# Kernel tuning notes

Hardware: AMD Instinct MI355X
Metric: run time of the kernel (lower is better)

The kernel has to match this reference:

```python
import jax, jax.numpy as jnp
import numpy as np

M, NQ, NKV, DX, DT = 8, 1024, 1024, 512, 2
H, HD = 8, 64            # num_heads, head_dim
INNER = H * HD           # 512
KHID = 16                # kernel MLP hidden dim
SCALE = HD ** -0.5


def setup_inputs() -> dict:
    key = jax.random.key(0)
    ks = jax.random.split(key, 16)
    s = lambda fan_in: 1.0 / np.sqrt(fan_in)
    return {
        "xq": jax.random.normal(ks[0], (M, NQ, DX), jnp.float32),
        "xk": jax.random.normal(ks[1], (M, NKV, DX), jnp.float32),
        "xv": jax.random.normal(ks[2], (M, NKV, DX), jnp.float32),
        "tq": jax.random.normal(ks[3], (M, NQ, DT), jnp.float32),
        "tk": jax.random.normal(ks[4], (M, NKV, DT), jnp.float32),
        # attention projections (bias=False for q/k/v, Linear bias for out)
        "w_q": jax.random.normal(ks[5], (DX, INNER), jnp.float32) * s(DX),
        "w_k": jax.random.normal(ks[6], (DX, INNER), jnp.float32) * s(DX),
        "w_v": jax.random.normal(ks[7], (DX, INNER), jnp.float32) * s(DX),
        "w_out": jax.random.normal(ks[8], (INNER, DX), jnp.float32) * s(INNER),
        "b_out": jnp.zeros((DX,), jnp.float32),
        # kernel MLP: dt -> KHID -> H (per-head pairwise bias)
        "kw1": jax.random.normal(ks[9], (DT, KHID), jnp.float32) * s(DT),
        "kb1": jnp.zeros((KHID,), jnp.float32),
        "kw2": jax.random.normal(ks[10], (KHID, H), jnp.float32) * s(KHID),
        "kb2": jnp.zeros((H,), jnp.float32),
    }


def reference(xq, xk, xv, tq, tk, w_q, w_k, w_v, w_out, b_out, kw1, kb1, kw2, kb2):
    # pairwise differences of input locations: [m, nq, nkv, dt]
    diff = tq[:, :, None, :] - tk[:, None, :, :]
    # kernel MLP -> per-head bias, rearranged to [m, h, nq, nkv]
    hmid = jax.nn.relu(diff @ kw1 + kb1)          # [m, nq, nkv, KHID]
    dots = jnp.einsum('mqkc,ch->mhqk', hmid, kw2) + kb2[None, :, None, None]
    # token attention: standard scaled QK scores
    q = (xq @ w_q).reshape(M, NQ, H, HD)          # [m, nq, h, d]
    k = (xk @ w_k).reshape(M, NKV, H, HD)
    token_dots = jnp.einsum('mqhd,mkhd->mhqk', q, k) * SCALE
    dots = dots + token_dots
    attn = jax.nn.softmax(dots, axis=-1)          # softmax over keys
    v = (xv @ w_v).reshape(M, NKV, H, HD)
    out = jnp.einsum('mhqk,mkhd->mqhd', attn, v).reshape(M, NQ, INNER)
    return out @ w_out + b_out                    # [m, nq, dx]
```

## Files before the change

kernel.cpp:

```cpp
#include <hip/hip_runtime.h>


typedef unsigned short u16;
typedef unsigned int   u32;
typedef short bf8 __attribute__((ext_vector_type(8)));
typedef float f4  __attribute__((ext_vector_type(4)));
typedef _Float16 h2 __attribute__((ext_vector_type(2)));

#define Mb 8
#define LOG2E 1.44269504088896f
#define SCALE2 (0.125f * LOG2E)
#define NTOK 4194304

__device__ __forceinline__ u16 f2bf(float f) {
    union { float f; u32 u; } v; v.f = f;
    u32 r = v.u + 0x7fffu + ((v.u >> 16) & 1u);
    return (u16)(r >> 16);
}
__device__ __forceinline__ u32 pk2(float a, float b) {
    u32 r;
    asm("v_cvt_pk_bf16_f32 %0, %1, %2" : "=v"(r) : "v"(a), "v"(b));
    return r;
}
__device__ __forceinline__ void gl_lds16(const u16* g, u16* l) {
    __builtin_amdgcn_global_load_lds(
        (const __attribute__((address_space(1))) u32*)g,
        (__attribute__((address_space(3))) u32*)l, 16, 0, 0);
}
__device__ __forceinline__ h2 h2_of(u32 x) {
    union { u32 u; h2 h; } c; c.u = x; return c.h;
}
__device__ __forceinline__ u32 u_of(h2 x) {
    union { h2 h; u32 u; } c; c.h = x; return c.u;
}
__device__ __forceinline__ float dot2(h2 a, h2 b, float c) {
#if __has_builtin(__builtin_amdgcn_fdot2)
    return __builtin_amdgcn_fdot2(a, b, c, false);
#else
    return fmaf((float)a[0], (float)b[0], fmaf((float)a[1], (float)b[1], c));
#endif
}

struct PArgs {
    const float* ws[4];
    u16* dstW;
};

__global__ __launch_bounds__(256) void prep(PArgs p) {
    __shared__ u16 tl[64][80];
    const int tid = threadIdx.x;
    const int bb = blockIdx.x;
    const int mat = bb >> 6, t = bb & 63;
    const int kt = t >> 3, nt = t & 7;
    const float* src = p.ws[mat] + (size_t)kt * 64 * 512 + (size_t)nt * 64;
    const int r0 = tid >> 4, c4 = (tid & 15) * 4;
    #pragma unroll
    for (int rr = 0; rr < 4; ++rr) {
        const int row = r0 + rr * 16;
        float4 a = *(const float4*)(src + (size_t)row * 512 + c4);
        tl[c4 + 0][row] = f2bf(a.x);
        tl[c4 + 1][row] = f2bf(a.y);
        tl[c4 + 2][row] = f2bf(a.z);
        tl[c4 + 3][row] = f2bf(a.w);
    }
    __syncthreads();
    u16* dst = p.dstW + (size_t)mat * 262144 + (size_t)nt * 64 * 512 + (size_t)kt * 64;
    #pragma unroll
    for (int i = 0; i < 2; ++i) {
        const int s2 = tid + i * 256;
        const int nrow = s2 >> 3, k8 = (s2 & 7) * 8;
        *(uint4*)(dst + (size_t)nrow * 512 + k8) = *(const uint4*)&tl[nrow][k8];
    }
}

struct GArgs {
    const void*  A[3];
    const u16*   W[3];
    void*        C[3];
    const float* bias;
    int          modeT[3];
    int          outf32;
    int          af32;
};

__global__ __launch_bounds__(256) void gemm_mfma(GArgs g) {
    __shared__ u16 Xs[128][32];
    __shared__ u16 Ws[128][32];

    const int z   = blockIdx.z;
    const int tid = threadIdx.x;
    const int w = tid >> 6, lane = tid & 63, quad = lane >> 4, l16 = lane & 15;
    const int wm = w >> 1, wn = w & 1;
    const int n0 = blockIdx.x * 128, t0 = blockIdx.y * 128;
    const int trans = g.modeT[z];

    f4 acc[4][4];
    #pragma unroll
    for (int i = 0; i < 4; ++i)
        #pragma unroll
        for (int j = 0; j < 4; ++j) acc[i][j] = (f4)0.f;

    const int lrow  = lane >> 2;
    const int kslot = (lane & 3) ^ ((lane >> 3) & 3);
    u16* ldsW0 = &Ws[w * 32][0];
    u16* ldsW1 = &Ws[w * 32 + 16][0];
    const u16* gW0 = g.W[z] + (size_t)(n0 + w * 32 + lrow) * 512 + kslot * 8;
    const u16* gW1 = gW0 + 16 * 512;

    u16* ldsX0 = &Xs[w * 32][0];
    u16* ldsX1 = &Xs[w * 32 + 16][0];
    const u16* gA0 = (const u16*)g.A[z] + (size_t)(t0 + w * 32 + lrow) * 512 + kslot * 8;
    const u16* gA1 = gA0 + 16 * 512;
    const int arow_s = tid >> 1, ah = tid & 1;
    const float* aF = (const float*)g.A[z] + (size_t)(t0 + arow_s) * 512 + ah * 16;
    const int s_sw = (arow_s >> 1) & 3;
    u16* aw0 = &Xs[arow_s][((2 * ah)     ^ s_sw) * 8];
    u16* aw1 = &Xs[arow_s][((2 * ah + 1) ^ s_sw) * 8];

    const int rslot = (quad ^ ((l16 >> 1) & 3)) * 8;

    for (int kc = 0; kc < 512; kc += 32) {
        __syncthreads();
        if (g.af32) {
            float4 f0 = *(const float4*)(aF + kc);
            float4 f1 = *(const float4*)(aF + kc + 4);
            float4 f2 = *(const float4*)(aF + kc + 8);
            float4 f3 = *(const float4*)(aF + kc + 12);
            uint4 v0, v1;
            v0.x = pk2(f0.x, f0.y); v0.y = pk2(f0.z, f0.w);
            v0.z = pk2(f1.x, f1.y); v0.w = pk2(f1.z, f1.w);
            v1.x = pk2(f2.x, f2.y); v1.y = pk2(f2.z, f2.w);
            v1.z = pk2(f3.x, f3.y); v1.w = pk2(f3.z, f3.w);
            *(uint4*)aw0 = v0;
            *(uint4*)aw1 = v1;
        } else {
            gl_lds16(gA0 + kc, ldsX0);
            gl_lds16(gA1 + kc, ldsX1);
        }
        gl_lds16(gW0 + kc, ldsW0);
        gl_lds16(gW1 + kc, ldsW1);
        __syncthreads();

        const u16* Abase = trans ? &Xs[0][0] : &Ws[0][0];
        const u16* Bbase = trans ? &Ws[0][0] : &Xs[0][0];
        const int arow = (trans ? wm : wn) * 64;
        const int brow = (trans ? wn : wm) * 64;
        bf8 af[4], bf[4];
        #pragma unroll
        for (int i = 0; i < 4; ++i)
            af[i] = *(const bf8*)(Abase + (arow + i * 16 + l16) * 32 + rslot);
        #pragma unroll
        for (int j = 0; j < 4; ++j)
            bf[j] = *(const bf8*)(Bbase + (brow + j * 16 + l16) * 32 + rslot);
        #pragma unroll
        for (int i = 0; i < 4; ++i)
            #pragma unroll
            for (int j = 0; j < 4; ++j)
                acc[i][j] = __builtin_amdgcn_mfma_f32_16x16x32_bf16(af[i], bf[j], acc[i][j], 0, 0, 0);
    }

    if (g.outf32) {
        float* Co = (float*)g.C[z];
        #pragma unroll
        for (int i = 0; i < 4; ++i) {
            const int nb = n0 + wn * 64 + i * 16 + quad * 4;
            float4 bv = *(const float4*)&g.bias[nb];
            #pragma unroll
            for (int j = 0; j < 4; ++j) {
                const int tok = t0 + wm * 64 + j * 16 + l16;
                float4 st;
                st.x = acc[i][j][0] + bv.x; st.y = acc[i][j][1] + bv.y;
                st.z = acc[i][j][2] + bv.z; st.w = acc[i][j][3] + bv.w;
                *(float4*)&Co[(size_t)tok * 512 + nb] = st;
            }
        }
    } else if (!trans) {
        u16* C = (u16*)g.C[z];
        #pragma unroll
        for (int i = 0; i < 4; ++i) {
            const int nb = n0 + wn * 64 + i * 16 + quad * 4;
            #pragma unroll
            for (int j = 0; j < 4; ++j) {
                const int tok = t0 + wm * 64 + j * 16 + l16;
                uint2 pw;
                pw.x = pk2(acc[i][j][0], acc[i][j][1]);
                pw.y = pk2(acc[i][j][2], acc[i][j][3]);
                *(uint2*)&C[(size_t)tok * 512 + nb] = pw;
            }
        }
    } else {
        u16* Vt = (u16*)g.C[z];
        #pragma unroll
        for (int i = 0; i < 4; ++i) {
            const int tokb = t0 + wm * 64 + i * 16 + quad * 4;
            const int mb = tokb >> 10, tb = tokb & 1023;
            #pragma unroll
            for (int j = 0; j < 4; ++j) {
                const int n = n0 + wn * 64 + j * 16 + l16;
                uint2 pw;
                pw.x = pk2(acc[i][j][0], acc[i][j][1]);
                pw.y = pk2(acc[i][j][2], acc[i][j][3]);
                *(uint2*)&Vt[(size_t)mb * 524288 + (size_t)n * 1024 + tb] = pw;
            }
        }
    }
}

__global__ __launch_bounds__(512) void attn_mfma(
    const u16* __restrict__ Q, const u16* __restrict__ K,
    const u16* __restrict__ Vt,
    const float* __restrict__ tqp, const float* __restrict__ tkp,
    const float* __restrict__ kw1, const float* __restrict__ kb1,
    const float* __restrict__ kw2,
    u16* __restrict__ O)
{
    __shared__ u16 sK[2][8][64][8];
    __shared__ u16 sV[2][8][64][8];
    __shared__ u32 sv2[2][8][68];
    __shared__ u16 sP[8][16][68];

    const int tid = threadIdx.x;
    const int w = tid >> 6, lane = tid & 63, quad = lane >> 4, l16 = lane & 15;
    const int b = (blockIdx.z * 8 + blockIdx.y) * 8 + blockIdx.x;
    const int xc = b & 7, j = b >> 3;
    const int hm = xc * 8 + (j & 7);
    const int qt = j >> 3;
    const int h = hm & 7, m = hm >> 3;
    const int q0 = qt * 128;
    const size_t qtok = (size_t)m * 1024 + q0 + w * 16 + l16;

    bf8 qf[2];
    {
        const u16* qp = Q + qtok * 512 + h * 64 + quad * 8;
        qf[0] = *(const bf8*)qp;
        qf[1] = *(const bf8*)(qp + 32);
    }
    h2 u2[8], w2p[8];
    {
        const float t0v = tqp[qtok * 2], t1v = tqp[qtok * 2 + 1];
        #pragma unroll
        for (int cp = 0; cp < 8; ++cp) {
            const int c0 = 2 * cp, c1 = 2 * cp + 1;
            float ua = fmaf(t0v, kw1[c0], fmaf(t1v, kw1[16 + c0], kb1[c0]));
            float ub = fmaf(t0v, kw1[c1], fmaf(t1v, kw1[16 + c1], kb1[c1]));
            u2[cp][0]  = (_Float16)ua;  u2[cp][1]  = (_Float16)ub;
            w2p[cp][0] = (_Float16)(LOG2E * kw2[c0 * 8 + h]);
            w2p[cp][1] = (_Float16)(LOG2E * kw2[c1 * 8 + h]);
        }
    }
    const float w0a = kw1[2 * w],     w1a = kw1[16 + 2 * w];
    const float w0b = kw1[2 * w + 1], w1b = kw1[16 + 2 * w + 1];

    const u16* gK = K + ((size_t)m * 1024 + lane) * 512 + h * 64 + w * 8;
    const u16* gV = Vt + (size_t)m * 524288 + (size_t)(h * 64 + lane) * 1024 + w * 8;
    const float* gT = tkp + (size_t)m * 2048 + lane * 2;

    float mrun = -1e30f, lrun = 0.f;
    f4 o[4];
    #pragma unroll
    for (int d = 0; d < 4; ++d) o[d] = (f4)0.f;

    auto STAGE = [&](int kt2, int nb) {
        const int k0n = kt2 * 64;
        float2 t = *(const float2*)(gT + k0n * 2);
        h2 pv;
        pv[0] = (_Float16)fmaf(t.x, w0a, t.y * w1a);
        pv[1] = (_Float16)fmaf(t.x, w0b, t.y * w1b);
        sv2[nb][w][lane] = u_of(pv);
        gl_lds16(gK + (size_t)k0n * 512, &sK[nb][w][0][0]);
        gl_lds16(gV + k0n,               &sV[nb][w][0][0]);
    };

    STAGE(0, 0);
    __syncthreads();

    int cur = 0;
    for (int kt = 0; kt < 16; ++kt) {
        if (kt < 15) STAGE(kt + 1, cur ^ 1);

        f4 s[4];
        #pragma unroll
        for (int msub = 0; msub < 4; ++msub) {
            bf8 kf0 = *(const bf8*)&sK[cur][quad][msub * 16 + l16][0];
            bf8 kf1 = *(const bf8*)&sK[cur][4 + quad][msub * 16 + l16][0];
            s[msub] = __builtin_amdgcn_mfma_f32_16x16x32_bf16(kf0, qf[0], (f4)0.f, 0, 0, 0);
            s[msub] = __builtin_amdgcn_mfma_f32_16x16x32_bf16(kf1, qf[1], s[msub], 0, 0, 0);
        }
        #pragma unroll
        for (int msub = 0; msub < 4; ++msub) {
            const int kb = msub * 16 + quad * 4;
            f4 b2 = (f4)0.f;
            #pragma unroll
            for (int cp = 0; cp < 8; ++cp) {
                uint4 vv = *(const uint4*)&sv2[cur][cp][kb];
                const h2 uc = u2[cp], wc = w2p[cp];
                const h2 z = (h2)(_Float16)0.f;
                h2 d0 = uc - h2_of(vv.x);
                h2 d1 = uc - h2_of(vv.y);
                h2 d2 = uc - h2_of(vv.z);
                h2 d3 = uc - h2_of(vv.w);
                d0 = __builtin_elementwise_max(d0, z);
                d1 = __builtin_elementwise_max(d1, z);
                d2 = __builtin_elementwise_max(d2, z);
                d3 = __builtin_elementwise_max(d3, z);
                b2[0] = dot2(d0, wc, b2[0]);
                b2[1] = dot2(d1, wc, b2[1]);
                b2[2] = dot2(d2, wc, b2[2]);
                b2[3] = dot2(d3, wc, b2[3]);
            }
            s[msub] = s[msub] * SCALE2 + b2;
        }
        float mx = -1e30f;
        #pragma unroll
        for (int msub = 0; msub < 4; ++msub) {
            mx = fmaxf(mx, fmaxf(fmaxf(s[msub][0], s[msub][1]),
                                 fmaxf(s[msub][2], s[msub][3])));
        }
        mx = fmaxf(mx, __shfl_xor(mx, 16));
        mx = fmaxf(mx, __shfl_xor(mx, 32));
        const float mnew = fmaxf(mrun, mx);
        float ps = 0.f;
        #pragma unroll
        for (int msub = 0; msub < 4; ++msub) {
            #pragma unroll
            for (int r = 0; r < 4; ++r) {
                float p = exp2f(s[msub][r] - mnew);
                s[msub][r] = p;
                ps += p;
            }
        }
        ps += __shfl_xor(ps, 16);
        ps += __shfl_xor(ps, 32);
        if (__all(mx <= mrun)) {
            lrun += ps;
        } else {
            const float alpha = exp2f(mrun - mnew);
            lrun = lrun * alpha + ps;
            mrun = mnew;
            #pragma unroll
            for (int d = 0; d < 4; ++d) o[d] = o[d] * alpha;
        }
        #pragma unroll
        for (int msub = 0; msub < 4; ++msub) {
            uint2 pw;
            pw.x = pk2(s[msub][0], s[msub][1]);
            pw.y = pk2(s[msub][2], s[msub][3]);
            *(uint2*)&sP[w][l16][msub * 16 + quad * 4] = pw;
        }
        #pragma unroll
        for (int dsub = 0; dsub < 4; ++dsub) {
            #pragma unroll
            for (int kc2 = 0; kc2 < 2; ++kc2) {
                bf8 vf = *(const bf8*)&sV[cur][kc2 * 4 + quad][dsub * 16 + l16][0];
                bf8 pf = *(const bf8*)&sP[w][l16][kc2 * 32 + quad * 8];
                o[dsub] = __builtin_amdgcn_mfma_f32_16x16x32_bf16(vf, pf, o[dsub], 0, 0, 0);
            }
        }

        if (kt < 15) __syncthreads();
        cur ^= 1;
    }

    const float inv = 1.f / lrun;
    #pragma unroll
    for (int dsub = 0; dsub < 4; ++dsub) {
        uint2 pw;
        pw.x = pk2(o[dsub][0] * inv, o[dsub][1] * inv);
        pw.y = pk2(o[dsub][2] * inv, o[dsub][3] * inv);
        *(uint2*)&O[qtok * 512 + h * 64 + dsub * 16 + quad * 4] = pw;
    }
}

extern "C" void kernel_launch(void* const* d_in, const int* in_sizes, int n_in,
                              void* d_out, int out_size, void* d_ws, size_t ws_size,
                              hipStream_t stream) {
    const float* xq    = (const float*)d_in[0];
    const float* xk    = (const float*)d_in[1];
    const float* xv    = (const float*)d_in[2];
    const float* tq    = (const float*)d_in[3];
    const float* tk    = (const float*)d_in[4];
    const float* w_q   = (const float*)d_in[5];
    const float* w_k   = (const float*)d_in[6];
    const float* w_v   = (const float*)d_in[7];
    const float* w_out = (const float*)d_in[8];
    const float* b_out = (const float*)d_in[9];
    const float* kw1   = (const float*)d_in[10];
    const float* kb1   = (const float*)d_in[11];
    const float* kw2   = (const float*)d_in[12];

    u16* Q  = (u16*)d_ws;
    u16* Kp = Q  + NTOK;
    u16* Vt = Kp + NTOK;
    u16* O  = Vt + NTOK;
    u16* Wq = O  + 3 * (size_t)NTOK;
    u16* Wk = Wq + 262144;
    u16* Wv = Wk + 262144;
    u16* Wo = Wv + 262144;

    PArgs p;
    p.ws[0] = w_q; p.ws[1] = w_k; p.ws[2] = w_v; p.ws[3] = w_out;
    p.dstW = Wq;
    prep<<<dim3(256), 256, 0, stream>>>(p);

    GArgs gq;
    gq.A[0] = xq;  gq.A[1] = xk;  gq.A[2] = xv;
    gq.W[0] = Wq;  gq.W[1] = Wk;  gq.W[2] = Wv;
    gq.C[0] = Q;   gq.C[1] = Kp;  gq.C[2] = Vt;
    gq.bias = nullptr;
    gq.modeT[0] = 0; gq.modeT[1] = 0; gq.modeT[2] = 1;
    gq.outf32 = 0; gq.af32 = 1;
    gemm_mfma<<<dim3(4, 64, 3), 256, 0, stream>>>(gq);

    attn_mfma<<<dim3(8, 8, Mb), 512, 0, stream>>>(Q, Kp, Vt, tq, tk,
                                                  kw1, kb1, kw2, O);

    GArgs go;
    go.A[0] = O;   go.A[1] = O;   go.A[2] = O;
    go.W[0] = Wo;  go.W[1] = Wo;  go.W[2] = Wo;
    go.C[0] = d_out; go.C[1] = d_out; go.C[2] = d_out;
    go.bias = b_out;
    go.modeT[0] = 0; go.modeT[1] = 0; go.modeT[2] = 0;
    go.outf32 = 1; go.af32 = 0;
    gemm_mfma<<<dim3(4, 64, 1), 256, 0, stream>>>(go);
}
```

Baseline: 259.7 us.

## Prefetch fp32 A tiles in GEMM and switch softmax to natural exp

The projection GEMM now loads the next k-chunk of fp32 activations into registers during the current iteration, so global load latency can overlap the LDS staging and MFMA work. The attention kernel drops the folded LOG2E scaling and calls __expf instead of exp2f, which likely adds a multiply per exponential. The workspace layout for the weight buffers is also compacted. The prefetch adds register pressure in the GEMM.

```diff
diff --git a/kernel.cpp b/kernel.cpp
--- a/kernel.cpp
+++ b/kernel.cpp
@@ -8,8 +8,7 @@
 typedef _Float16 h2 __attribute__((ext_vector_type(2)));
 
 #define Mb 8
-#define LOG2E 1.44269504088896f
-#define SCALE2 (0.125f * LOG2E)
+#define SCALE 0.125f
 #define NTOK 4194304
 
 __device__ __forceinline__ u16 f2bf(float f) {
@@ -49,8 +48,8 @@
 __global__ __launch_bounds__(256) void prep(PArgs p) {
     __shared__ u16 tl[64][80];
     const int tid = threadIdx.x;
-    const int bb = blockIdx.x;
-    const int mat = bb >> 6, t = bb & 63;
+    const int b = blockIdx.x;
+    const int mat = b >> 6, t = b & 63;
     const int kt = t >> 3, nt = t & 7;
     const float* src = p.ws[mat] + (size_t)kt * 64 * 512 + (size_t)nt * 64;
     const int r0 = tid >> 4, c4 = (tid & 15) * 4;
@@ -111,6 +110,7 @@
     u16* ldsX1 = &Xs[w * 32 + 16][0];
     const u16* gA0 = (const u16*)g.A[z] + (size_t)(t0 + w * 32 + lrow) * 512 + kslot * 8;
     const u16* gA1 = gA0 + 16 * 512;
+
     const int arow_s = tid >> 1, ah = tid & 1;
     const float* aF = (const float*)g.A[z] + (size_t)(t0 + arow_s) * 512 + ah * 16;
     const int s_sw = (arow_s >> 1) & 3;
@@ -119,13 +119,17 @@
 
     const int rslot = (quad ^ ((l16 >> 1) & 3)) * 8;
 
+    float4 f0, f1, f2, f3;
+    if (g.af32) {
+        f0 = *(const float4*)(aF + 0);
+        f1 = *(const float4*)(aF + 4);
+        f2 = *(const float4*)(aF + 8);
+        f3 = *(const float4*)(aF + 12);
+    }
+
     for (int kc = 0; kc < 512; kc += 32) {
         __syncthreads();
         if (g.af32) {
-            float4 f0 = *(const float4*)(aF + kc);
-            float4 f1 = *(const float4*)(aF + kc + 4);
-            float4 f2 = *(const float4*)(aF + kc + 8);
-            float4 f3 = *(const float4*)(aF + kc + 12);
             uint4 v0, v1;
             v0.x = pk2(f0.x, f0.y); v0.y = pk2(f0.z, f0.w);
             v0.z = pk2(f1.x, f1.y); v0.w = pk2(f1.z, f1.w);
@@ -139,6 +143,12 @@
         }
         gl_lds16(gW0 + kc, ldsW0);
         gl_lds16(gW1 + kc, ldsW1);
+        if (g.af32 && kc + 32 < 512) {
+            f0 = *(const float4*)(aF + kc + 32);
+            f1 = *(const float4*)(aF + kc + 36);
+            f2 = *(const float4*)(aF + kc + 40);
+            f3 = *(const float4*)(aF + kc + 44);
+        }
         __syncthreads();
 
         const u16* Abase = trans ? &Xs[0][0] : &Ws[0][0];
@@ -243,9 +253,8 @@
             const int c0 = 2 * cp, c1 = 2 * cp + 1;
             float ua = fmaf(t0v, kw1[c0], fmaf(t1v, kw1[16 + c0], kb1[c0]));
             float ub = fmaf(t0v, kw1[c1], fmaf(t1v, kw1[16 + c1], kb1[c1]));
-            u2[cp][0]  = (_Float16)ua;  u2[cp][1]  = (_Float16)ub;
-            w2p[cp][0] = (_Float16)(LOG2E * kw2[c0 * 8 + h]);
-            w2p[cp][1] = (_Float16)(LOG2E * kw2[c1 * 8 + h]);
+            u2[cp][0]  = (_Float16)ua;              u2[cp][1]  = (_Float16)ub;
+            w2p[cp][0] = (_Float16)kw2[c0 * 8 + h]; w2p[cp][1] = (_Float16)kw2[c1 * 8 + h];
         }
     }
     const float w0a = kw1[2 * w],     w1a = kw1[16 + 2 * w];
@@ -308,7 +317,7 @@
                 b2[2] = dot2(d2, wc, b2[2]);
                 b2[3] = dot2(d3, wc, b2[3]);
             }
-            s[msub] = s[msub] * SCALE2 + b2;
+            s[msub] = s[msub] * SCALE + b2;
         }
         float mx = -1e30f;
         #pragma unroll
@@ -324,7 +333,7 @@
         for (int msub = 0; msub < 4; ++msub) {
             #pragma unroll
             for (int r = 0; r < 4; ++r) {
-                float p = exp2f(s[msub][r] - mnew);
+                float p = __expf(s[msub][r] - mnew);
                 s[msub][r] = p;
                 ps += p;
             }
@@ -334,7 +343,7 @@
         if (__all(mx <= mrun)) {
             lrun += ps;
         } else {
-            const float alpha = exp2f(mrun - mnew);
+            const float alpha = __expf(mrun - mnew);
             lrun = lrun * alpha + ps;
             mrun = mnew;
             #pragma unroll
@@ -392,7 +401,7 @@
     u16* Kp = Q  + NTOK;
     u16* Vt = Kp + NTOK;
     u16* O  = Vt + NTOK;
-    u16* Wq = O  + 3 * (size_t)NTOK;
+    u16* Wq = O  + NTOK;
     u16* Wk = Wq + 262144;
     u16* Wv = Wk + 262144;
     u16* Wo = Wv + 262144;
```

Measured after the change: 248.2 us. 4.4% less time.
